# Optimization experiments

Hardware: AMD Instinct MI355X
Metric: run time of the kernel (lower is better)

The kernel has to match this reference:

```python
import jax, jax.numpy as jnp
import numpy as np

D = 128
N = 100000
E = 500000
DIM_OUT = 2


def setup_inputs() -> dict:
    key = jax.random.key(0)
    ks = jax.random.split(key, 12)
    s = lambda d: 1.0 / np.sqrt(d)
    return {
        "x": jax.random.normal(ks[0], (N, D), jnp.float32),
        "edge_attr": jax.random.normal(ks[1], (E, D), jnp.float32),
        # node head MLP: D -> D -> DIM_OUT
        "W1": jax.random.uniform(ks[2], (D, D), jnp.float32, -s(D), s(D)),
        "b1": jnp.zeros((D,), jnp.float32),
        "W2": jax.random.uniform(ks[3], (D, DIM_OUT), jnp.float32, -s(D), s(D)),
        "b2": jnp.zeros((DIM_OUT,), jnp.float32),
        # edge aux head MLP: 3D -> 3D -> 1
        "V1": jax.random.uniform(ks[4], (3 * D, 3 * D), jnp.float32, -s(3 * D), s(3 * D)),
        "bv1": jnp.zeros((3 * D,), jnp.float32),
        "V2": jax.random.uniform(ks[5], (3 * D, 1), jnp.float32, -s(3 * D), s(3 * D)),
        "bv2": jnp.zeros((1,), jnp.float32),
        "edge_combine_weight": jnp.asarray(0.5, jnp.float32),
        "edge_index": jax.random.randint(ks[6], (2, E), 0, N, jnp.int64),
        "y": jax.random.randint(ks[7], (N,), 0, 2, jnp.int64),
        "batch_size": 50000,
    }


def reference(x, edge_attr, W1, b1, W2, b2, V1, bv1, V2, bv2,
              edge_combine_weight, edge_index, y, batch_size):
    # node classification head: 2-layer MLP
    node_logits = jax.nn.relu(x @ W1 + b1) @ W2 + b2  # [N, 2]

    src, dst = edge_index[0], edge_index[1]
    # gather src/dst node embeddings, concat edge attrs -> [E, 3D]
    edge_input = jnp.concatenate([x[src], x[dst], edge_attr], axis=-1)
    edge_scores = (jax.nn.relu(edge_input @ V1 + bv1) @ V2 + bv2)[:, 0]  # [E]
    edge_sig = jax.nn.sigmoid(edge_scores)

    # scatter-max into node slots; empty slots -> 0 (torch_scatter semantics)
    signal = jax.ops.segment_max(edge_sig, src, num_segments=N)
    signal = jnp.where(jnp.isfinite(signal), signal, 0.0)

    node_logits = node_logits.at[:, 1].add(edge_combine_weight * signal)

    pred = node_logits[:batch_size]
    label = y[:batch_size]
    return pred, label
```

## Files before the change

### kernel.cpp

```cpp
#include <hip/hip_runtime.h>
#include <hip/hip_bf16.h>

typedef __bf16 bf16;
typedef bf16 bf16x8 __attribute__((ext_vector_type(8)));
typedef float f32x4 __attribute__((ext_vector_type(4)));

#define D 128

__global__ void prep_kernel(const float* __restrict__ V1, const float* __restrict__ W1,
                            bf16* __restrict__ V1t, bf16* __restrict__ W1t) {
  int i = blockIdx.x * 256 + threadIdx.x;
  if (i < 384 * 384) { int k = i / 384, n = i % 384; V1t[n * 384 + k] = (bf16)V1[i]; }
  if (i < 128 * 128) { int k = i >> 7, n = i & 127;  W1t[n * 128 + k] = (bf16)W1[i]; }
}

__global__ void compact_kernel(const int* __restrict__ ei, int E, int bs,
                               int* __restrict__ count, int* __restrict__ list) {
  int e = blockIdx.x * 256 + threadIdx.x;
  if (e < E && ei[e] < bs) {
    int p = atomicAdd(count, 1);
    list[p] = e;
  }
}

__global__ __launch_bounds__(256, 2) void node_kernel(
    const float* __restrict__ x, const bf16* __restrict__ W1t,
    const float* __restrict__ b1, const float* __restrict__ W2,
    const float* __restrict__ b2, float* __restrict__ logits, int bs)
{
  __shared__ bf16 sA[64][136];
  __shared__ float sOut0[64], sOut1[64];

  int tid = threadIdx.x;
  if (tid < 64) { sOut0[tid] = 0.f; sOut1[tid] = 0.f; }

  {
    int g = tid >> 5, fl = tid & 31;
#pragma unroll
    for (int i = 0; i < 8; ++i) {
      int row = i * 8 + g;
      const float4* base = (const float4*)(x + (size_t)(blockIdx.x * 64 + row) * D);
      float4 v = base[fl];
      union { bf16 h[4]; uint2 u; } cv;
      cv.h[0] = (bf16)v.x; cv.h[1] = (bf16)v.y; cv.h[2] = (bf16)v.z; cv.h[3] = (bf16)v.w;
      *(uint2*)&sA[row][fl * 4] = cv.u;
    }
  }
  __syncthreads();

  int wave = tid >> 6, lane = tid & 63;
  int l15 = lane & 15, quad = lane >> 4;

  f32x4 acc[2][4];
#pragma unroll
  for (int ct = 0; ct < 2; ++ct)
#pragma unroll
    for (int rt = 0; rt < 4; ++rt)
      acc[ct][rt] = (f32x4){0.f, 0.f, 0.f, 0.f};

  for (int kc = 0; kc < 4; ++kc) {
    int k = kc * 32 + quad * 8;
    bf16x8 a[4], b[2];
#pragma unroll
    for (int rt = 0; rt < 4; ++rt)
      a[rt] = *(const bf16x8*)&sA[rt * 16 + l15][k];
#pragma unroll
    for (int ct = 0; ct < 2; ++ct)
      b[ct] = *(const bf16x8*)&W1t[(size_t)(wave * 32 + ct * 16 + l15) * 128 + k];
#pragma unroll
    for (int ct = 0; ct < 2; ++ct)
#pragma unroll
      for (int rt = 0; rt < 4; ++rt)
        acc[ct][rt] = __builtin_amdgcn_mfma_f32_16x16x32_bf16(a[rt], b[ct], acc[ct][rt], 0, 0, 0);
  }

  float bc[2], w0[2], w1[2];
#pragma unroll
  for (int ct = 0; ct < 2; ++ct) {
    int n = wave * 32 + ct * 16 + l15;
    bc[ct] = b1[n]; w0[ct] = W2[n * 2]; w1[ct] = W2[n * 2 + 1];
  }
#pragma unroll
  for (int rt = 0; rt < 4; ++rt) {
#pragma unroll
    for (int reg = 0; reg < 4; ++reg) {
      float p0 = 0.f, p1 = 0.f;
#pragma unroll
      for (int ct = 0; ct < 2; ++ct) {
        float h = fmaxf(acc[ct][rt][reg] + bc[ct], 0.f);
        p0 += h * w0[ct]; p1 += h * w1[ct];
      }
      p0 += __shfl_xor(p0, 1, 16); p0 += __shfl_xor(p0, 2, 16);
      p0 += __shfl_xor(p0, 4, 16); p0 += __shfl_xor(p0, 8, 16);
      p1 += __shfl_xor(p1, 1, 16); p1 += __shfl_xor(p1, 2, 16);
      p1 += __shfl_xor(p1, 4, 16); p1 += __shfl_xor(p1, 8, 16);
      if (l15 == 0) {
        int row = rt * 16 + quad * 4 + reg;
        atomicAdd(&sOut0[row], p0);
        atomicAdd(&sOut1[row], p1);
      }
    }
  }
  __syncthreads();
  if (tid < 64) {
    int node = blockIdx.x * 64 + tid;
    if (node < bs) {
      logits[2 * node]     = sOut0[tid] + b2[0];
      logits[2 * node + 1] = sOut1[tid] + b2[1];
    }
  }
}

__global__ __launch_bounds__(256, 2) void edge_kernel(
    const float* __restrict__ x, const float* __restrict__ ea,
    const bf16* __restrict__ V1t, const float* __restrict__ bv1,
    const float* __restrict__ V2, const float* __restrict__ bv2,
    const int* __restrict__ ei, const int* __restrict__ count,
    const int* __restrict__ list, float* __restrict__ signal,
    int E, int bs)
{
  __shared__ bf16 sA[64][392];
  __shared__ float sScore[64];
  __shared__ int sSrc[64], sDst[64], sE[64];

  int nvalid = *count - (int)(blockIdx.x * 64);
  if (nvalid <= 0) return;
  if (nvalid > 64) nvalid = 64;

  int tid = threadIdx.x;
  if (tid < 64) {
    int e = 0;
    if (tid < nvalid) e = list[blockIdx.x * 64 + tid];
    sE[tid] = e;
    sSrc[tid] = ei[e];
    sDst[tid] = ei[E + e];
    sScore[tid] = 0.f;
  }
  __syncthreads();

  {
    int g = tid >> 5, fl = tid & 31;
#pragma unroll
    for (int i = 0; i < 24; ++i) {
      int t = i * 8 + g;
      int row = t & 63, seg = t >> 6;
      const float* base;
      if (seg == 0)      base = x  + (size_t)sSrc[row] * D;
      else if (seg == 1) base = x  + (size_t)sDst[row] * D;
      else               base = ea + (size_t)sE[row]   * D;
      float4 v = ((const float4*)base)[fl];
      union { bf16 h[4]; uint2 u; } cv;
      cv.h[0] = (bf16)v.x; cv.h[1] = (bf16)v.y; cv.h[2] = (bf16)v.z; cv.h[3] = (bf16)v.w;
      *(uint2*)&sA[row][seg * 128 + fl * 4] = cv.u;
    }
  }
  __syncthreads();

  int wave = tid >> 6, lane = tid & 63;
  int l15 = lane & 15, quad = lane >> 4;

  f32x4 acc[6][4];
#pragma unroll
  for (int ct = 0; ct < 6; ++ct)
#pragma unroll
    for (int rt = 0; rt < 4; ++rt)
      acc[ct][rt] = (f32x4){0.f, 0.f, 0.f, 0.f};

  const bf16* Bbase = V1t + (size_t)(wave * 96 + l15) * 384 + quad * 8;

  for (int kc = 0; kc < 12; ++kc) {
    int k = kc * 32 + quad * 8;
    bf16x8 a[4], b[6];
#pragma unroll
    for (int rt = 0; rt < 4; ++rt)
      a[rt] = *(const bf16x8*)&sA[rt * 16 + l15][k];
#pragma unroll
    for (int ct = 0; ct < 6; ++ct)
      b[ct] = *(const bf16x8*)(Bbase + (size_t)ct * 16 * 384 + kc * 32);
#pragma unroll
    for (int ct = 0; ct < 6; ++ct)
#pragma unroll
      for (int rt = 0; rt < 4; ++rt)
        acc[ct][rt] = __builtin_amdgcn_mfma_f32_16x16x32_bf16(a[rt], b[ct], acc[ct][rt], 0, 0, 0);
  }

  float bvc[6], v2c[6];
#pragma unroll
  for (int ct = 0; ct < 6; ++ct) {
    int n = wave * 96 + ct * 16 + l15;
    bvc[ct] = bv1[n]; v2c[ct] = V2[n];
  }
#pragma unroll
  for (int rt = 0; rt < 4; ++rt) {
#pragma unroll
    for (int reg = 0; reg < 4; ++reg) {
      float p = 0.f;
#pragma unroll
      for (int ct = 0; ct < 6; ++ct)
        p += fmaxf(acc[ct][rt][reg] + bvc[ct], 0.f) * v2c[ct];
      p += __shfl_xor(p, 1, 16);
      p += __shfl_xor(p, 2, 16);
      p += __shfl_xor(p, 4, 16);
      p += __shfl_xor(p, 8, 16);
      if (l15 == 0)
        atomicAdd(&sScore[rt * 16 + quad * 4 + reg], p);
    }
  }
  __syncthreads();
  if (tid < nvalid) {
    float sc = sScore[tid] + bv2[0];
    float sig = 1.f / (1.f + __expf(-sc));
    atomicMax((int*)&signal[sSrc[tid]], __float_as_int(sig));
  }
}

__global__ void combine_kernel(const float* __restrict__ logits, const float* __restrict__ signal,
                               const int* __restrict__ y, const float* __restrict__ ecw,
                               float* __restrict__ out, int bs) {
  int i = blockIdx.x * 256 + threadIdx.x;
  if (i < bs) {
    out[2 * i]     = logits[2 * i];
    out[2 * i + 1] = logits[2 * i + 1] + ecw[0] * signal[i];
    out[2 * bs + i] = (float)y[i];
  }
}

extern "C" void kernel_launch(void* const* d_in, const int* in_sizes, int n_in,
                              void* d_out, int out_size, void* d_ws, size_t ws_size,
                              hipStream_t stream) {
  const float* x   = (const float*)d_in[0];
  const float* ea  = (const float*)d_in[1];
  const float* W1  = (const float*)d_in[2];
  const float* b1  = (const float*)d_in[3];
  const float* W2  = (const float*)d_in[4];
  const float* b2  = (const float*)d_in[5];
  const float* V1  = (const float*)d_in[6];
  const float* bv1 = (const float*)d_in[7];
  const float* V2  = (const float*)d_in[8];
  const float* bv2 = (const float*)d_in[9];
  const float* ecw = (const float*)d_in[10];
  const int*   ei  = (const int*)d_in[11];
  const int*   y   = (const int*)d_in[12];

  int E  = in_sizes[1] / D;
  int bs = out_size / 3;

  char* ws = (char*)d_ws;
  size_t off = 0;
  bf16* V1t = (bf16*)(ws + off); off += (size_t)384 * 384 * 2;
  bf16* W1t = (bf16*)(ws + off); off += (size_t)128 * 128 * 2;
  float* signal = (float*)(ws + off); off += (size_t)bs * 4;
  float* logits = (float*)(ws + off); off += (size_t)bs * 8;
  int* count = (int*)(ws + off); off += 16;
  int* list  = (int*)(ws + off); off += (size_t)E * 4;

  hipMemsetAsync(signal, 0, (size_t)bs * 4, stream);
  hipMemsetAsync(count, 0, 4, stream);

  prep_kernel<<<(384 * 384 + 255) / 256, 256, 0, stream>>>(V1, W1, V1t, W1t);
  compact_kernel<<<(E + 255) / 256, 256, 0, stream>>>(ei, E, bs, count, list);
  node_kernel<<<(bs + 63) / 64, 256, 0, stream>>>(x, W1t, b1, W2, b2, logits, bs);
  edge_kernel<<<(E + 63) / 64, 256, 0, stream>>>(x, ea, V1t, bv1, V2, bv2,
                                                 ei, count, list, signal, E, bs);
  combine_kernel<<<(bs + 255) / 256, 256, 0, stream>>>(logits, signal, y, ecw,
                                                       (float*)d_out, bs);
}
```

Measured before the change: 686.4 us.

## Split edge kernel into gather-pack pass and LDS-direct bf16 GEMM pass

The edge MLP is split in two. A pack kernel gathers the src, dst and edge_attr rows, converts them to bf16 and writes swizzled 64-row tiles to workspace. A GEMM kernel then streams each tile into LDS with global_load_lds and runs MFMA. Prep, compact and signal zeroing are merged into one kernel, which drops a memset and a launch. The split adds an extra write and read of the packed tiles and needs enough workspace, otherwise it falls back to the fused kernel.

```diff
diff --git a/kernel.cpp b/kernel.cpp
--- a/kernel.cpp
+++ b/kernel.cpp
@@ -1,5 +1,6 @@
 #include <hip/hip_runtime.h>
 #include <hip/hip_bf16.h>
+#include <stdint.h>
 
 typedef __bf16 bf16;
 typedef bf16 bf16x8 __attribute__((ext_vector_type(8)));
@@ -7,19 +8,18 @@
 
 #define D 128
 
-__global__ void prep_kernel(const float* __restrict__ V1, const float* __restrict__ W1,
-                            bf16* __restrict__ V1t, bf16* __restrict__ W1t) {
+__global__ void prep_compact_kernel(const float* __restrict__ V1, const float* __restrict__ W1,
+                                    bf16* __restrict__ V1t, bf16* __restrict__ W1t,
+                                    const int* __restrict__ ei, int E, int bs,
+                                    int* __restrict__ count, int* __restrict__ list,
+                                    float* __restrict__ signal) {
   int i = blockIdx.x * 256 + threadIdx.x;
   if (i < 384 * 384) { int k = i / 384, n = i % 384; V1t[n * 384 + k] = (bf16)V1[i]; }
   if (i < 128 * 128) { int k = i >> 7, n = i & 127;  W1t[n * 128 + k] = (bf16)W1[i]; }
-}
-
-__global__ void compact_kernel(const int* __restrict__ ei, int E, int bs,
-                               int* __restrict__ count, int* __restrict__ list) {
-  int e = blockIdx.x * 256 + threadIdx.x;
-  if (e < E && ei[e] < bs) {
+  if (i < bs) signal[i] = 0.f;
+  if (i < E && ei[i] < bs) {
     int p = atomicAdd(count, 1);
-    list[p] = e;
+    list[p] = i;
   }
 }
 
@@ -108,6 +108,150 @@
       logits[2 * node]     = sOut0[tid] + b2[0];
       logits[2 * node + 1] = sOut1[tid] + b2[1];
     }
+  }
+}
+
+__global__ __launch_bounds__(256) void pack_kernel(
+    const float* __restrict__ x, const float* __restrict__ ea,
+    const int* __restrict__ ei, const int* __restrict__ count,
+    const int* __restrict__ list, bf16* __restrict__ packed, int E)
+{
+  __shared__ int sSrc[64], sDst[64], sE[64];
+  int nvalid = *count - (int)(blockIdx.x * 64);
+  if (nvalid <= 0) return;
+  if (nvalid > 64) nvalid = 64;
+
+  int tid = threadIdx.x;
+  if (tid < 64) {
+    int e = 0;
+    if (tid < nvalid) e = list[blockIdx.x * 64 + tid];
+    sE[tid] = e; sSrc[tid] = ei[e]; sDst[tid] = ei[E + e];
+  }
+  __syncthreads();
+
+  char* out = (char*)packed + (size_t)blockIdx.x * 49152;
+  int g = tid >> 5, fl = tid & 31;
+
+#pragma unroll
+  for (int half = 0; half < 2; ++half) {
+    float4 buf[12];
+#pragma unroll
+    for (int j = 0; j < 12; ++j) {
+      int t = (half * 12 + j) * 8 + g;
+      int row = t & 63, seg = t >> 6;
+      const float* base;
+      if (seg == 0)      base = x  + (size_t)sSrc[row] * D;
+      else if (seg == 1) base = x  + (size_t)sDst[row] * D;
+      else               base = ea + (size_t)sE[row]   * D;
+      buf[j] = ((const float4*)base)[fl];
+    }
+#pragma unroll
+    for (int j = 0; j < 12; ++j) {
+      int t = (half * 12 + j) * 8 + g;
+      int row = t & 63, seg = t >> 6;
+      union { bf16 h[4]; uint2 u; } cv;
+      cv.h[0] = (bf16)buf[j].x; cv.h[1] = (bf16)buf[j].y;
+      cv.h[2] = (bf16)buf[j].z; cv.h[3] = (bf16)buf[j].w;
+      int off = (row * 768 + seg * 256 + fl * 8) ^ ((row & 7) << 4);
+      *(uint2*)(out + off) = cv.u;
+    }
+  }
+}
+
+__global__ __launch_bounds__(256, 2) void edge_gemm_kernel(
+    const bf16* __restrict__ packed, const bf16* __restrict__ V1t,
+    const float* __restrict__ bv1, const float* __restrict__ V2,
+    const float* __restrict__ bv2, const int* __restrict__ ei,
+    const int* __restrict__ count, const int* __restrict__ list,
+    float* __restrict__ signal, int E)
+{
+  __shared__ __align__(16) char sA[49152];
+  __shared__ float sScore[64];
+  __shared__ int sSrc[64];
+
+  int nvalid = *count - (int)(blockIdx.x * 64);
+  if (nvalid <= 0) return;
+  if (nvalid > 64) nvalid = 64;
+
+  int tid = threadIdx.x;
+  int wave = tid >> 6, lane = tid & 63;
+
+  const char* tileb = (const char*)packed + (size_t)blockIdx.x * 49152;
+#pragma unroll
+  for (int i = 0; i < 12; ++i) {
+    int off = i * 4096 + wave * 1024;
+    __builtin_amdgcn_global_load_lds(
+        (const __attribute__((address_space(1))) unsigned int*)(tileb + off + lane * 16),
+        (__attribute__((address_space(3))) unsigned int*)(sA + off),
+        16, 0, 0);
+  }
+
+  if (tid < 64) {
+    sScore[tid] = 0.f;
+    int e = (tid < nvalid) ? list[blockIdx.x * 64 + tid] : 0;
+    sSrc[tid] = ei[e];
+  }
+
+  asm volatile("s_waitcnt vmcnt(0)" ::: "memory");
+  __syncthreads();
+
+  int l15 = lane & 15, quad = lane >> 4;
+  int xr = (l15 & 7) << 4;
+
+  f32x4 acc[6][4];
+#pragma unroll
+  for (int ct = 0; ct < 6; ++ct)
+#pragma unroll
+    for (int rt = 0; rt < 4; ++rt)
+      acc[ct][rt] = (f32x4){0.f, 0.f, 0.f, 0.f};
+
+  const bf16* Bbase = V1t + (size_t)(wave * 96 + l15) * 384 + quad * 8;
+
+  for (int kc = 0; kc < 12; ++kc) {
+    bf16x8 a[4], b[6];
+#pragma unroll
+    for (int rt = 0; rt < 4; ++rt) {
+      int row = rt * 16 + l15;
+      int off = (row * 768 + kc * 64 + quad * 16) ^ xr;
+      a[rt] = *(const bf16x8*)(sA + off);
+    }
+#pragma unroll
+    for (int ct = 0; ct < 6; ++ct)
+      b[ct] = *(const bf16x8*)(Bbase + (size_t)ct * 16 * 384 + kc * 32);
+#pragma unroll
+    for (int ct = 0; ct < 6; ++ct)
+#pragma unroll
+      for (int rt = 0; rt < 4; ++rt)
+        acc[ct][rt] = __builtin_amdgcn_mfma_f32_16x16x32_bf16(a[rt], b[ct], acc[ct][rt], 0, 0, 0);
+  }
+
+  float bvc[6], v2c[6];
+#pragma unroll
+  for (int ct = 0; ct < 6; ++ct) {
+    int n = wave * 96 + ct * 16 + l15;
+    bvc[ct] = bv1[n]; v2c[ct] = V2[n];
+  }
+#pragma unroll
+  for (int rt = 0; rt < 4; ++rt) {
+#pragma unroll
+    for (int reg = 0; reg < 4; ++reg) {
+      float p = 0.f;
+#pragma unroll
+      for (int ct = 0; ct < 6; ++ct)
+        p += fmaxf(acc[ct][rt][reg] + bvc[ct], 0.f) * v2c[ct];
+      p += __shfl_xor(p, 1, 16);
+      p += __shfl_xor(p, 2, 16);
+      p += __shfl_xor(p, 4, 16);
+      p += __shfl_xor(p, 8, 16);
+      if (l15 == 0)
+        atomicAdd(&sScore[rt * 16 + quad * 4 + reg], p);
+    }
+  }
+  __syncthreads();
+  if (tid < nvalid) {
+    float sc = sScore[tid] + bv2[0];
+    float sig = 1.f / (1.f + __expf(-sc));
+    atomicMax((int*)&signal[sSrc[tid]], __float_as_int(sig));
   }
 }
 
@@ -247,21 +391,37 @@
 
   char* ws = (char*)d_ws;
   size_t off = 0;
+  auto rnd16 = [](size_t v) { return (v + 15) & ~(size_t)15; };
   bf16* V1t = (bf16*)(ws + off); off += (size_t)384 * 384 * 2;
   bf16* W1t = (bf16*)(ws + off); off += (size_t)128 * 128 * 2;
-  float* signal = (float*)(ws + off); off += (size_t)bs * 4;
-  float* logits = (float*)(ws + off); off += (size_t)bs * 8;
+  float* signal = (float*)(ws + off); off += rnd16((size_t)bs * 4);
+  float* logits = (float*)(ws + off); off += rnd16((size_t)bs * 8);
   int* count = (int*)(ws + off); off += 16;
-  int* list  = (int*)(ws + off); off += (size_t)E * 4;
-
-  hipMemsetAsync(signal, 0, (size_t)bs * 4, stream);
+  int* list  = (int*)(ws + off); off += rnd16((size_t)E * 4);
+
+  int ntiles = (E + 63) / 64;
+  bf16* packed = (bf16*)(ws + off);
+  size_t need = off + (size_t)ntiles * 49152;
+  bool split = (ws_size >= need);
+
   hipMemsetAsync(count, 0, 4, stream);
 
-  prep_kernel<<<(384 * 384 + 255) / 256, 256, 0, stream>>>(V1, W1, V1t, W1t);
-  compact_kernel<<<(E + 255) / 256, 256, 0, stream>>>(ei, E, bs, count, list);
-  node_kernel<<<(bs + 63) / 64, 256, 0, stream>>>(x, W1t, b1, W2, b2, logits, bs);
-  edge_kernel<<<(E + 63) / 64, 256, 0, stream>>>(x, ea, V1t, bv1, V2, bv2,
-                                                 ei, count, list, signal, E, bs);
+  int maxi = E;
+  if (384 * 384 > maxi) maxi = 384 * 384;
+  if (bs > maxi) maxi = bs;
+  prep_compact_kernel<<<(maxi + 255) / 256, 256, 0, stream>>>(
+      V1, W1, V1t, W1t, ei, E, bs, count, list, signal);
+
+  if (split) {
+    pack_kernel<<<ntiles, 256, 0, stream>>>(x, ea, ei, count, list, packed, E);
+    edge_gemm_kernel<<<ntiles, 256, 0, stream>>>(packed, V1t, bv1, V2, bv2,
+                                                 ei, count, list, signal, E);
+    node_kernel<<<(bs + 63) / 64, 256, 0, stream>>>(x, W1t, b1, W2, b2, logits, bs);
+  } else {
+    node_kernel<<<(bs + 63) / 64, 256, 0, stream>>>(x, W1t, b1, W2, b2, logits, bs);
+    edge_kernel<<<ntiles, 256, 0, stream>>>(x, ea, V1t, bv1, V2, bv2,
+                                            ei, count, list, signal, E, bs);
+  }
   combine_kernel<<<(bs + 255) / 256, 256, 0, stream>>>(logits, signal, y, ecw,
                                                        (float*)d_out, bs);
 }
```

New measurement: 724.4 us. 1.06x slower.

## Make edge GEMM persistent with LDS-resident swizzled V1 halves

Applied to the files above, without the earlier changes.

Replaces the per-tile edge kernel with a persistent 256-block kernel. Each block loads one 192-column half of a pre-swizzled bf16 V1 into LDS once via global_load_lds, then loops over 32-row edge tiles, gathering A operands straight from global memory into registers. Partial scores from the two column halves are accumulated into a global score array with atomics, and a separate finalize kernel applies sigmoid and the scatter-max. The prep and compact kernels are fused and the memset of signal is dropped. This removes repeated V1 reads from global memory per tile, in exchange for duplicated gathers across the two halves, global atomics, and an extra kernel launch.

```diff
diff --git a/kernel.cpp b/kernel.cpp
--- a/kernel.cpp
+++ b/kernel.cpp
@@ -1,5 +1,6 @@
 #include <hip/hip_runtime.h>
 #include <hip/hip_bf16.h>
+#include <stdint.h>
 
 typedef __bf16 bf16;
 typedef bf16 bf16x8 __attribute__((ext_vector_type(8)));
@@ -7,19 +8,25 @@
 
 #define D 128
 
-__global__ void prep_kernel(const float* __restrict__ V1, const float* __restrict__ W1,
-                            bf16* __restrict__ V1t, bf16* __restrict__ W1t) {
+__global__ void prep_compact_kernel(const float* __restrict__ V1, const float* __restrict__ W1,
+                                    bf16* __restrict__ V1p, bf16* __restrict__ W1t,
+                                    const int* __restrict__ ei, int E, int bs,
+                                    int* __restrict__ count, int* __restrict__ list,
+                                    float* __restrict__ signal, float* __restrict__ score) {
   int i = blockIdx.x * 256 + threadIdx.x;
-  if (i < 384 * 384) { int k = i / 384, n = i % 384; V1t[n * 384 + k] = (bf16)V1[i]; }
+  if (i < 384 * 384) {
+    int k = i / 384, n = i % 384;
+    int c = (n >= 192) ? 1 : 0;
+    int nl = n - c * 192;
+    int off = c * 147456 + ((nl * 768 + k * 2) ^ ((nl & 7) << 4));
+    *(bf16*)((char*)V1p + off) = (bf16)V1[i];
+  }
   if (i < 128 * 128) { int k = i >> 7, n = i & 127;  W1t[n * 128 + k] = (bf16)W1[i]; }
-}
-
-__global__ void compact_kernel(const int* __restrict__ ei, int E, int bs,
-                               int* __restrict__ count, int* __restrict__ list) {
-  int e = blockIdx.x * 256 + threadIdx.x;
-  if (e < E && ei[e] < bs) {
+  if (i < bs) signal[i] = 0.f;
+  if (i < E + 64) score[i] = 0.f;
+  if (i < E && ei[i] < bs) {
     int p = atomicAdd(count, 1);
-    list[p] = e;
+    list[p] = i;
   }
 }
 
@@ -111,106 +118,130 @@
   }
 }
 
-__global__ __launch_bounds__(256, 2) void edge_kernel(
+__global__ __launch_bounds__(512, 2) void edge_gemm_kernel(
     const float* __restrict__ x, const float* __restrict__ ea,
-    const bf16* __restrict__ V1t, const float* __restrict__ bv1,
-    const float* __restrict__ V2, const float* __restrict__ bv2,
-    const int* __restrict__ ei, const int* __restrict__ count,
-    const int* __restrict__ list, float* __restrict__ signal,
-    int E, int bs)
+    const bf16* __restrict__ V1p, const float* __restrict__ bv1,
+    const float* __restrict__ V2, const int* __restrict__ ei,
+    const int* __restrict__ count, const int* __restrict__ list,
+    float* __restrict__ score, int E)
 {
-  __shared__ bf16 sA[64][392];
-  __shared__ float sScore[64];
-  __shared__ int sSrc[64], sDst[64], sE[64];
-
-  int nvalid = *count - (int)(blockIdx.x * 64);
-  if (nvalid <= 0) return;
-  if (nvalid > 64) nvalid = 64;
+  __shared__ __align__(16) char sB[147456];
 
   int tid = threadIdx.x;
-  if (tid < 64) {
-    int e = 0;
-    if (tid < nvalid) e = list[blockIdx.x * 64 + tid];
-    sE[tid] = e;
-    sSrc[tid] = ei[e];
-    sDst[tid] = ei[E + e];
-    sScore[tid] = 0.f;
-  }
-  __syncthreads();
-
-  {
-    int g = tid >> 5, fl = tid & 31;
-#pragma unroll
-    for (int i = 0; i < 24; ++i) {
-      int t = i * 8 + g;
-      int row = t & 63, seg = t >> 6;
-      const float* base;
-      if (seg == 0)      base = x  + (size_t)sSrc[row] * D;
-      else if (seg == 1) base = x  + (size_t)sDst[row] * D;
-      else               base = ea + (size_t)sE[row]   * D;
-      float4 v = ((const float4*)base)[fl];
-      union { bf16 h[4]; uint2 u; } cv;
-      cv.h[0] = (bf16)v.x; cv.h[1] = (bf16)v.y; cv.h[2] = (bf16)v.z; cv.h[3] = (bf16)v.w;
-      *(uint2*)&sA[row][seg * 128 + fl * 4] = cv.u;
-    }
-  }
-  __syncthreads();
-
   int wave = tid >> 6, lane = tid & 63;
   int l15 = lane & 15, quad = lane >> 4;
-
-  f32x4 acc[6][4];
-#pragma unroll
-  for (int ct = 0; ct < 6; ++ct)
-#pragma unroll
-    for (int rt = 0; rt < 4; ++rt)
-      acc[ct][rt] = (f32x4){0.f, 0.f, 0.f, 0.f};
-
-  const bf16* Bbase = V1t + (size_t)(wave * 96 + l15) * 384 + quad * 8;
-
-  for (int kc = 0; kc < 12; ++kc) {
-    int k = kc * 32 + quad * 8;
-    bf16x8 a[4], b[6];
-#pragma unroll
-    for (int rt = 0; rt < 4; ++rt)
-      a[rt] = *(const bf16x8*)&sA[rt * 16 + l15][k];
-#pragma unroll
-    for (int ct = 0; ct < 6; ++ct)
-      b[ct] = *(const bf16x8*)(Bbase + (size_t)ct * 16 * 384 + kc * 32);
-#pragma unroll
-    for (int ct = 0; ct < 6; ++ct)
-#pragma unroll
-      for (int rt = 0; rt < 4; ++rt)
-        acc[ct][rt] = __builtin_amdgcn_mfma_f32_16x16x32_bf16(a[rt], b[ct], acc[ct][rt], 0, 0, 0);
-  }
-
-  float bvc[6], v2c[6];
-#pragma unroll
-  for (int ct = 0; ct < 6; ++ct) {
-    int n = wave * 96 + ct * 16 + l15;
+  int chunk = blockIdx.x & 1;
+
+  const char* bsrc = (const char*)V1p + (size_t)chunk * 147456;
+#pragma unroll
+  for (int i = 0; i < 18; ++i) {
+    int off = i * 8192 + wave * 1024;
+    __builtin_amdgcn_global_load_lds(
+        (const __attribute__((address_space(1))) unsigned int*)(bsrc + off + lane * 16),
+        (__attribute__((address_space(3))) unsigned int*)(sB + off),
+        16, 0, 0);
+  }
+
+  int cnt = *count;
+
+  float bvc[12], v2c[12];
+#pragma unroll
+  for (int ct = 0; ct < 12; ++ct) {
+    int n = chunk * 192 + ct * 16 + l15;
     bvc[ct] = bv1[n]; v2c[ct] = V2[n];
   }
-#pragma unroll
-  for (int rt = 0; rt < 4; ++rt) {
-#pragma unroll
-    for (int reg = 0; reg < 4; ++reg) {
-      float p = 0.f;
-#pragma unroll
-      for (int ct = 0; ct < 6; ++ct)
-        p += fmaxf(acc[ct][rt][reg] + bvc[ct], 0.f) * v2c[ct];
-      p += __shfl_xor(p, 1, 16);
-      p += __shfl_xor(p, 2, 16);
-      p += __shfl_xor(p, 4, 16);
-      p += __shfl_xor(p, 8, 16);
-      if (l15 == 0)
-        atomicAdd(&sScore[rt * 16 + quad * 4 + reg], p);
-    }
-  }
+
+  asm volatile("s_waitcnt vmcnt(0)" ::: "memory");
   __syncthreads();
-  if (tid < nvalid) {
-    float sc = sScore[tid] + bv2[0];
+
+  int ntiles = (cnt + 63) >> 6;
+  int nunits = ntiles * 2;
+  int worker = (int)(blockIdx.x >> 1) * 8 + wave;
+  int xr = (l15 & 7) << 4;
+
+  for (int u = worker; u < nunits; u += 1024) {
+    int tile = u >> 1, half = u & 1;
+    int rowbase = tile * 64 + half * 32;
+
+    int pr0 = rowbase + l15;
+    int pr1 = pr0 + 16;
+    int e0 = (pr0 < cnt) ? list[pr0] : 0;
+    int e1 = (pr1 < cnt) ? list[pr1] : 0;
+    int s0 = ei[e0], d0 = ei[E + e0];
+    int s1 = ei[e1], d1 = ei[E + e1];
+    const float* xs0 = x + (size_t)s0 * D;
+    const float* xd0 = x + (size_t)d0 * D;
+    const float* pe0 = ea + (size_t)e0 * D;
+    const float* xs1 = x + (size_t)s1 * D;
+    const float* xd1 = x + (size_t)d1 * D;
+    const float* pe1 = ea + (size_t)e1 * D;
+
+    f32x4 acc[12][2];
+#pragma unroll
+    for (int ct = 0; ct < 12; ++ct) {
+      acc[ct][0] = (f32x4){0.f, 0.f, 0.f, 0.f};
+      acc[ct][1] = (f32x4){0.f, 0.f, 0.f, 0.f};
+    }
+
+#pragma unroll
+    for (int kc = 0; kc < 12; ++kc) {
+      const int seg = kc >> 2;
+      int kf = (kc & 3) * 32 + quad * 8;
+      const float* base0 = (seg == 0) ? xs0 : (seg == 1) ? xd0 : pe0;
+      const float* base1 = (seg == 0) ? xs1 : (seg == 1) ? xd1 : pe1;
+
+      float4 v0a = *(const float4*)(base0 + kf);
+      float4 v0b = *(const float4*)(base0 + kf + 4);
+      float4 v1a = *(const float4*)(base1 + kf);
+      float4 v1b = *(const float4*)(base1 + kf + 4);
+
+      union { bf16 h[8]; bf16x8 v; } ca, cb;
+      ca.h[0] = (bf16)v0a.x; ca.h[1] = (bf16)v0a.y; ca.h[2] = (bf16)v0a.z; ca.h[3] = (bf16)v0a.w;
+      ca.h[4] = (bf16)v0b.x; ca.h[5] = (bf16)v0b.y; ca.h[6] = (bf16)v0b.z; ca.h[7] = (bf16)v0b.w;
+      cb.h[0] = (bf16)v1a.x; cb.h[1] = (bf16)v1a.y; cb.h[2] = (bf16)v1a.z; cb.h[3] = (bf16)v1a.w;
+      cb.h[4] = (bf16)v1b.x; cb.h[5] = (bf16)v1b.y; cb.h[6] = (bf16)v1b.z; cb.h[7] = (bf16)v1b.w;
+      bf16x8 a0 = ca.v, a1 = cb.v;
+
+      bf16x8 b[12];
+#pragma unroll
+      for (int ct = 0; ct < 12; ++ct) {
+        int off = ((ct * 16 + l15) * 768 + kc * 64 + quad * 16) ^ xr;
+        b[ct] = *(const bf16x8*)(sB + off);
+      }
+#pragma unroll
+      for (int ct = 0; ct < 12; ++ct) {
+        acc[ct][0] = __builtin_amdgcn_mfma_f32_16x16x32_bf16(a0, b[ct], acc[ct][0], 0, 0, 0);
+        acc[ct][1] = __builtin_amdgcn_mfma_f32_16x16x32_bf16(a1, b[ct], acc[ct][1], 0, 0, 0);
+      }
+    }
+
+#pragma unroll
+    for (int rt = 0; rt < 2; ++rt) {
+#pragma unroll
+      for (int reg = 0; reg < 4; ++reg) {
+        float p = 0.f;
+#pragma unroll
+        for (int ct = 0; ct < 12; ++ct)
+          p += fmaxf(acc[ct][rt][reg] + bvc[ct], 0.f) * v2c[ct];
+        p += __shfl_xor(p, 1, 16);
+        p += __shfl_xor(p, 2, 16);
+        p += __shfl_xor(p, 4, 16);
+        p += __shfl_xor(p, 8, 16);
+        if (l15 == 0)
+          atomicAdd(&score[rowbase + rt * 16 + quad * 4 + reg], p);
+      }
+    }
+  }
+}
+
+__global__ void finalize_kernel(const float* __restrict__ score, const int* __restrict__ count,
+                                const int* __restrict__ list, const int* __restrict__ ei,
+                                const float* __restrict__ bv2, float* __restrict__ signal) {
+  int p = blockIdx.x * 256 + threadIdx.x;
+  if (p < *count) {
+    float sc = score[p] + bv2[0];
     float sig = 1.f / (1.f + __expf(-sc));
-    atomicMax((int*)&signal[sSrc[tid]], __float_as_int(sig));
+    atomicMax((int*)&signal[ei[list[p]]], __float_as_int(sig));
   }
 }
 
@@ -247,21 +278,27 @@
 
   char* ws = (char*)d_ws;
   size_t off = 0;
-  bf16* V1t = (bf16*)(ws + off); off += (size_t)384 * 384 * 2;
+  auto rnd16 = [](size_t v) { return (v + 15) & ~(size_t)15; };
+  bf16* V1p = (bf16*)(ws + off); off += (size_t)2 * 147456;
   bf16* W1t = (bf16*)(ws + off); off += (size_t)128 * 128 * 2;
-  float* signal = (float*)(ws + off); off += (size_t)bs * 4;
-  float* logits = (float*)(ws + off); off += (size_t)bs * 8;
+  float* signal = (float*)(ws + off); off += rnd16((size_t)bs * 4);
+  float* logits = (float*)(ws + off); off += rnd16((size_t)bs * 8);
   int* count = (int*)(ws + off); off += 16;
-  int* list  = (int*)(ws + off); off += (size_t)E * 4;
-
-  hipMemsetAsync(signal, 0, (size_t)bs * 4, stream);
+  int* list  = (int*)(ws + off); off += rnd16((size_t)E * 4);
+  float* score = (float*)(ws + off); off += rnd16((size_t)(E + 64) * 4);
+
   hipMemsetAsync(count, 0, 4, stream);
 
-  prep_kernel<<<(384 * 384 + 255) / 256, 256, 0, stream>>>(V1, W1, V1t, W1t);
-  compact_kernel<<<(E + 255) / 256, 256, 0, stream>>>(ei, E, bs, count, list);
+  int maxi = E + 64;
+  if (384 * 384 > maxi) maxi = 384 * 384;
+  if (bs > maxi) maxi = bs;
+  prep_compact_kernel<<<(maxi + 255) / 256, 256, 0, stream>>>(
+      V1, W1, V1p, W1t, ei, E, bs, count, list, signal, score);
+
+  edge_gemm_kernel<<<256, 512, 0, stream>>>(x, ea, V1p, bv1, V2,
+                                            ei, count, list, score, E);
   node_kernel<<<(bs + 63) / 64, 256, 0, stream>>>(x, W1t, b1, W2, b2, logits, bs);
-  edge_kernel<<<(E + 63) / 64, 256, 0, stream>>>(x, ea, V1t, bv1, V2, bv2,
-                                                 ei, count, list, signal, E, bs);
+  finalize_kernel<<<(E + 255) / 256, 256, 0, stream>>>(score, count, list, ei, bv2, signal);
   combine_kernel<<<(bs + 255) / 256, 256, 0, stream>>>(logits, signal, y, ecw,
                                                        (float*)d_out, bs);
 }
```

New measurement: 972.0 us. 1.42x slower.
